# Kernel optimization log

Hardware: AMD Instinct MI355X
Metric: run time of the kernel (lower is better)

Reference implementation:

```python
import jax, jax.numpy as jnp
import numpy as np

BN_EPS = 1e-5


def cond_conv(x, att_w, att_b, weight, pad):
    """CondConv: per-sample expert-mixed conv.
    x: [N,C,H,W]; att_w: [K,C]; att_b: [K]; weight: [K,O,I,kh,kw]; pad: (ph,pw)."""
    pooled = x.mean(axis=(2, 3))                         # [N,C]  (AdaptiveAvgPool2d(1))
    att = jax.nn.sigmoid(pooled @ att_w.T + att_b)       # [N,K]  (1x1 conv + sigmoid)
    agg_w = jnp.einsum('nk,koihw->noihw', att, weight)   # per-sample kernels [N,O,I,kh,kw]

    def conv1(xi, wi):
        return jax.lax.conv_general_dilated(
            xi[None], wi, window_strides=(1, 1),
            padding=[(pad[0], pad[0]), (pad[1], pad[1])],
            dimension_numbers=('NCHW', 'OIHW', 'NCHW'))[0]

    return jax.vmap(conv1)(x, agg_w)                     # [N,O,H,W]


def batchnorm(x, gamma, beta):
    # training-mode BN: biased batch stats over (N,H,W)
    mean = x.mean(axis=(0, 2, 3), keepdims=True)
    var = x.var(axis=(0, 2, 3), keepdims=True)
    xn = (x - mean) * jax.lax.rsqrt(var + BN_EPS)
    return xn * gamma[None, :, None, None] + beta[None, :, None, None]


def channel_shuffle(x, g):
    N, C, H, W = x.shape
    return x.reshape(N, g, C // g, H, W).transpose(0, 2, 1, 3, 4).reshape(N, C, H, W)


def setup_inputs() -> dict:
    key = jax.random.key(0)
    ks = jax.random.split(key, 8)
    N, C, H, W = 32, 256, 64, 64
    Cb, K = C // 4, 4
    inp = {
        'x': jax.random.normal(ks[0], (N, C, H, W), jnp.float32),
        'sq_att_w': jax.random.normal(ks[1], (K, Cb), jnp.float32) * 0.1,
        'sq_att_b': jnp.zeros((K,), jnp.float32),
        'sq_w': jax.random.normal(ks[2], (K, Cb, Cb, 3, 3), jnp.float32) * 0.05,
        'sq_g': jnp.ones((Cb,), jnp.float32),
        'sq_b': jnp.zeros((Cb,), jnp.float32),
        'ver_att_w': jax.random.normal(ks[3], (K, Cb), jnp.float32) * 0.1,
        'ver_att_b': jnp.zeros((K,), jnp.float32),
        'ver_w': jax.random.normal(ks[4], (K, Cb, Cb, 3, 1), jnp.float32) * 0.05,
        'ver_g': jnp.ones((Cb,), jnp.float32),
        'ver_b': jnp.zeros((Cb,), jnp.float32),
        'hor_att_w': jax.random.normal(ks[5], (K, Cb), jnp.float32) * 0.1,
        'hor_att_b': jnp.zeros((K,), jnp.float32),
        'hor_w': jax.random.normal(ks[6], (K, Cb, Cb, 1, 3), jnp.float32) * 0.05,
        'hor_g': jnp.ones((Cb,), jnp.float32),
        'hor_b': jnp.zeros((Cb,), jnp.float32),
    }
    return inp


def reference(x, sq_att_w, sq_att_b, sq_w, sq_g, sq_b,
              ver_att_w, ver_att_b, ver_w, ver_g, ver_b,
              hor_att_w, hor_att_b, hor_w, hor_g, hor_b):
    # q_Split: chunk into 4 along channels
    s0, s1, s2, s3 = jnp.split(x, 4, axis=1)
    # square branch: CondConv 3x3 pad 1 + BN
    sq = batchnorm(cond_conv(s1, sq_att_w, sq_att_b, sq_w, (1, 1)), sq_g, sq_b)
    # vertical branch: CondConv 3x1 pad (1,0) + BN (crop layer is Identity since offset=0)
    ve = batchnorm(cond_conv(s2, ver_att_w, ver_att_b, ver_w, (1, 0)), ver_g, ver_b)
    # horizontal branch: CondConv 1x3 pad (0,1) + BN
    ho = batchnorm(cond_conv(s3, hor_att_w, hor_att_b, hor_w, (0, 1)), hor_g, hor_b)
    out = jnp.concatenate((s0, sq, ve, ho), axis=1)
    return channel_shuffle(out, 8)
```

## Files before the change

### kernel.cpp

```cpp
#include <hip/hip_runtime.h>
#include <cstddef>
#include <cstdint>


typedef __attribute__((ext_vector_type(8))) short frag8;
typedef __attribute__((ext_vector_type(16))) float accf16;

#define HW 4096
#define CNT_INV (1.0f / 131072.0f)
#define CSTR 1056
#define RSTR 8448
#define XT_BR (32ull * 66 * 8448)

#define WS_POOLED 0
#define WS_SS     6528
#define WS_PST    6912
#define WS_WBF_SQ  203520
#define WS_WBF_VER 793344
#define WS_WBF_HOR 989952
#define WS_XT      1186560

__device__ __forceinline__ int shuf_ch(int c) { return ((c & 31) << 3) | (c >> 5); }

__device__ __forceinline__ unsigned bf16pair(float a, float b) {
    unsigned ua = __builtin_bit_cast(unsigned, a);
    unsigned ub = __builtin_bit_cast(unsigned, b);
    ua = (ua + 0x7fffu + ((ua >> 16) & 1u)) >> 16;
    ub = (ub + 0x7fffu + ((ub >> 16) & 1u)) >> 16;
    return ua | (ub << 16);
}

__device__ __forceinline__ void gload_lds16(const void* g, void* l) {
    __builtin_amdgcn_global_load_lds(
        (const __attribute__((address_space(1))) void*)g,
        (__attribute__((address_space(3))) void*)l, 16, 0, 0);
}

__global__ void __launch_bounds__(256) prepass_kernel(
    const float* __restrict__ x, unsigned char* __restrict__ xt,
    float* __restrict__ pooled) {
    const int bid = blockIdx.x;
    const int c8 = bid & 7;
    const int n = (bid >> 3) & 31;
    const int b = bid >> 8;
    const int tid = threadIdx.x;
    const int w = tid & 63, q = tid >> 6;
    const float* xb = x + (size_t)(n * 256 + 64 * (b + 1) + c8 * 8) * HW;
    unsigned char* xtb = xt + (size_t)b * XT_BR + (size_t)n * 66 * RSTR + c8 * CSTR;

    float ps[8] = {0.f, 0.f, 0.f, 0.f, 0.f, 0.f, 0.f, 0.f};
    for (int h = q; h < 64; h += 4) {
        float v[8];
#pragma unroll
        for (int j = 0; j < 8; ++j) v[j] = xb[(size_t)j * HW + h * 64 + w];
        unsigned pk[4];
#pragma unroll
        for (int j = 0; j < 4; ++j) pk[j] = bf16pair(v[2 * j], v[2 * j + 1]);
        *(uint4*)(xtb + (size_t)(h + 1) * RSTR + (w + 1) * 16) = *(uint4*)pk;
#pragma unroll
        for (int j = 0; j < 8; ++j) ps[j] += v[j];
    }
    for (int idx = tid; idx < 260; idx += 256) {
        int p, slot;
        if (idx < 66)       { p = 0;         slot = idx; }
        else if (idx < 132) { p = 65;        slot = idx - 66; }
        else if (idx < 196) { p = idx - 131; slot = 0; }
        else                { p = idx - 195; slot = 65; }
        *(uint4*)(xtb + (size_t)p * RSTR + slot * 16) = uint4{0, 0, 0, 0};
    }
    __shared__ float red[4][8];
#pragma unroll
    for (int j = 0; j < 8; ++j)
#pragma unroll
        for (int off = 32; off; off >>= 1) ps[j] += __shfl_down(ps[j], off, 64);
    if ((tid & 63) == 0)
#pragma unroll
        for (int j = 0; j < 8; ++j) red[q][j] = ps[j];
    __syncthreads();
    if (tid < 8)
        pooled[(b * 32 + n) * 64 + c8 * 8 + tid] =
            (red[0][tid] + red[1][tid] + red[2][tid] + red[3][tid]) * (1.f / 4096.f);
}

template <int TAPS>
__device__ __forceinline__ void aggbf_body(const float* __restrict__ w,
                                           const float* __restrict__ pooled_b,
                                           const float* __restrict__ aw,
                                           const float* __restrict__ ab,
                                           unsigned* __restrict__ wbf, int bid) {
    const int tid = threadIdx.x;
    int idx = bid * 256 + tid;
    int ip = idx & 31;
    int o  = (idx >> 5) & 63;
    int t  = (idx >> 11) % TAPS;
    int n  = (idx >> 11) / TAPS;

    __shared__ float satt[4];
    if (tid < 64) {
        float p = pooled_b[n * 64 + tid];
#pragma unroll
        for (int k = 0; k < 4; ++k) {
            float v = p * aw[k * 64 + tid];
#pragma unroll
            for (int off = 32; off; off >>= 1) v += __shfl_down(v, off, 64);
            if (tid == 0) satt[k] = 1.f / (1.f + expf(-(v + ab[k])));
        }
    }
    __syncthreads();
    const float a0 = satt[0], a1 = satt[1], a2 = satt[2], a3 = satt[3];

    constexpr int PS = 64 * 64 * TAPS;
    int base = (o * 64 + ip * 2) * TAPS + t;
    float v0 = a0*w[base] + a1*w[PS+base] + a2*w[2*PS+base] + a3*w[3*PS+base];
    int base1 = base + TAPS;
    float v1 = a0*w[base1] + a1*w[PS+base1] + a2*w[2*PS+base1] + a3*w[3*PS+base1];
    int f = ip >> 2, jj = ip & 3;
    wbf[(((n * TAPS + t) * 8 + f) * 64 + o) * 4 + jj] = bf16pair(v0, v1);
}

__global__ void __launch_bounds__(256) aggbf_all_kernel(
    const float* __restrict__ pooled,
    const float* __restrict__ aw0, const float* __restrict__ ab0,
    const float* __restrict__ aw1, const float* __restrict__ ab1,
    const float* __restrict__ aw2, const float* __restrict__ ab2,
    const float* __restrict__ sq_w, const float* __restrict__ ver_w,
    const float* __restrict__ hor_w,
    unsigned* __restrict__ wsq, unsigned* __restrict__ wver,
    unsigned* __restrict__ whor) {
    int bid = blockIdx.x;
    if (bid < 2304)
        aggbf_body<9>(sq_w, pooled, aw0, ab0, wsq, bid);
    else if (bid < 3072)
        aggbf_body<3>(ver_w, pooled + 2048, aw1, ab1, wver, bid - 2304);
    else
        aggbf_body<3>(hor_w, pooled + 4096, aw2, ab2, whor, bid - 3072);
}

#define LOADA(dst, tt) \
    _Pragma("unroll") for (int kk = 0; kk < 4; ++kk) { \
        dst[kk]     = wp[(tt) * 512 + kk * 128]; \
        dst[4 + kk] = wp[(tt) * 512 + kk * 128 + 32]; \
    }

#define TAPSTEP(tt, CUR) { \
    const int r_ = (tt) / KW, dw_ = (tt) % KW - PW; \
    const unsigned char* bp_ = xs + (rh * 2 + r_) * RSTR + hi * CSTR + \
                               (wcol + dw_ + 1) * 16; \
    _Pragma("unroll") for (int kk = 0; kk < 4; ++kk) { \
        frag8 b0 = *(const frag8*)(bp_ + kk * 2 * CSTR); \
        frag8 b1 = *(const frag8*)(bp_ + kk * 2 * CSTR + RSTR); \
        a00 = __builtin_amdgcn_mfma_f32_32x32x16_bf16(CUR[kk],     b0, a00, 0, 0, 0); \
        a10 = __builtin_amdgcn_mfma_f32_32x32x16_bf16(CUR[4 + kk], b0, a10, 0, 0, 0); \
        a01 = __builtin_amdgcn_mfma_f32_32x32x16_bf16(CUR[kk],     b1, a01, 0, 0, 0); \
        a11 = __builtin_amdgcn_mfma_f32_32x32x16_bf16(CUR[4 + kk], b1, a11, 0, 0, 0); \
    } }

template <int KH, int KW, int PH, int PW>
__device__ __forceinline__ void conv_body(
    const unsigned char* __restrict__ xt, const unsigned* __restrict__ wbf,
    float* __restrict__ out, float* __restrict__ pst, int cbase, int bid,
    unsigned char* xs, float (*red1)[2][2][16], float (*red2)[2][2][16]) {
    constexpr int TAPS = KH * KW;
    constexpr int HB = 4;
    constexpr int ROWS = HB + KH - 1;
    constexpr int TOT = ROWS * RSTR;
    constexpr int NCH = (TOT + 1023) >> 10;
    const int hb = bid & 15, n = bid >> 4;
    const int h0 = hb * HB;
    const int tid = threadIdx.x;
    const int lane = tid & 63;
    const int wv = tid >> 6;
    const int rh = wv >> 1, wn = wv & 1;
    const int l31 = lane & 31, hi = lane >> 5;
    const int wcol = wn * 32 + l31;

    {
        const unsigned char* src = xt +
            (size_t)(n * 66 + h0 + (KH == 1 ? 1 : 0)) * RSTR + lane * 16;
#pragma unroll
        for (int c = wv; c < NCH; c += 4)
            gload_lds16(src + (c << 10), xs + (c << 10));
    }

    const frag8* wp = (const frag8*)wbf + (size_t)n * TAPS * 512 + hi * 64 + l31;

    frag8 aA[8], aB[8];
    LOADA(aA, 0);
    __syncthreads();

    accf16 a00 = {}, a01 = {}, a10 = {}, a11 = {};
#pragma unroll
    for (int t = 0; t < TAPS; t += 2) {
        if (t + 1 < TAPS) LOADA(aB, t + 1);
        TAPSTEP(t, aA);
        if (t + 2 < TAPS) LOADA(aA, t + 2);
        if (t + 1 < TAPS) TAPSTEP(t + 1, aB);
    }

    {
        float* ob = out + (size_t)n * 256 * HW + (h0 + rh * 2) * 64 + wcol;
#pragma unroll
        for (int rg = 0; rg < 16; ++rg) {
            const int o = (rg & 3) + 8 * (rg >> 2) + 4 * hi;
            float* p0 = ob + (size_t)shuf_ch(cbase + o) * HW;
            p0[0]  = a00[rg];
            p0[64] = a01[rg];
            float* p1 = ob + (size_t)shuf_ch(cbase + 32 + o) * HW;
            p1[0]  = a10[rg];
            p1[64] = a11[rg];
        }
    }

#pragma unroll
    for (int rg = 0; rg < 16; ++rg) {
        float u1 = a00[rg] + a01[rg];
        float u2 = a00[rg] * a00[rg] + a01[rg] * a01[rg];
        float w1 = a10[rg] + a11[rg];
        float w2 = a10[rg] * a10[rg] + a11[rg] * a11[rg];
#pragma unroll
        for (int off = 16; off; off >>= 1) {
            u1 += __shfl_down(u1, off, 32);
            u2 += __shfl_down(u2, off, 32);
            w1 += __shfl_down(w1, off, 32);
            w2 += __shfl_down(w2, off, 32);
        }
        if (l31 == 0) {
            red1[wv][0][hi][rg] = u1; red2[wv][0][hi][rg] = u2;
            red1[wv][1][hi][rg] = w1; red2[wv][1][hi][rg] = w2;
        }
    }
    __syncthreads();
    if (tid < 64) {
        const int rg = tid & 15, hi2 = (tid >> 4) & 1, wm2 = tid >> 5;
        float s1 = 0.f, s2 = 0.f;
#pragma unroll
        for (int v = 0; v < 4; ++v) {
            s1 += red1[v][wm2][hi2][rg];
            s2 += red2[v][wm2][hi2][rg];
        }
        const int o = wm2 * 32 + (rg & 3) + 8 * (rg >> 2) + 4 * hi2;
        const int slot = n * 16 + hb;
        pst[o * 1024 + slot] = s1;
        pst[o * 1024 + 512 + slot] = s2;
    }
}

__device__ __forceinline__ void s0_body(const float* __restrict__ x,
                                        float* __restrict__ out, int bid) {
    const int n = bid >> 4, c0 = (bid & 15) * 4, tid = threadIdx.x;
#pragma unroll
    for (int j = 0; j < 4; ++j) {
        const int c = c0 + j;
        const float4* s = (const float4*)(x + (size_t)(n * 256 + c) * HW);
        float4* d = (float4*)(out + (size_t)(n * 256 + shuf_ch(c)) * HW);
#pragma unroll
        for (int it = 0; it < 4; ++it) d[tid + it * 256] = s[tid + it * 256];
    }
}

__global__ void __launch_bounds__(256, 3) conv_all_kernel(
    const float* __restrict__ x, const unsigned char* __restrict__ xt,
    const unsigned* __restrict__ wsq, const unsigned* __restrict__ wver,
    const unsigned* __restrict__ whor,
    float* __restrict__ out, float* __restrict__ pst) {
    __shared__ __align__(16) unsigned char xs[6 * RSTR + 512];
    __shared__ float red1[4][2][2][16], red2[4][2][2][16];
    int bid = blockIdx.x;
    if (bid < 512)
        conv_body<3, 3, 1, 1>(xt, wsq, out, pst, 64, bid, xs, red1, red2);
    else if (bid < 1024)
        conv_body<3, 1, 1, 0>(xt + XT_BR, wver, out, pst + 65536, 128,
                              bid - 512, xs, red1, red2);
    else if (bid < 1536)
        conv_body<1, 3, 0, 1>(xt + 2 * XT_BR, whor, out, pst + 131072, 192,
                              bid - 1024, xs, red1, red2);
    else
        s0_body(x, out, bid - 1536);
}

__global__ void __launch_bounds__(256) bnstats_all_kernel(
    const float* __restrict__ pst,
    const float* __restrict__ g0, const float* __restrict__ b0,
    const float* __restrict__ g1, const float* __restrict__ b1,
    const float* __restrict__ g2, const float* __restrict__ b2,
    float* __restrict__ ss) {
    int br = blockIdx.x >> 6, o = blockIdx.x & 63, t = threadIdx.x;
    const float* gamma = (br == 0) ? g0 : (br == 1) ? g1 : g2;
    const float* beta  = (br == 0) ? b0 : (br == 1) ? b1 : b2;
    const float* p = pst + br * 65536 + o * 1024;
    float s1 = 0.f, s2 = 0.f;
    for (int i = t; i < 512; i += 256) {
        s1 += p[i];
        s2 += p[512 + i];
    }
#pragma unroll
    for (int off = 32; off; off >>= 1) {
        s1 += __shfl_down(s1, off, 64);
        s2 += __shfl_down(s2, off, 64);
    }
    __shared__ float r1[4], r2[4];
    if ((t & 63) == 0) { r1[t >> 6] = s1; r2[t >> 6] = s2; }
    __syncthreads();
    if (t == 0) {
        float S1 = r1[0] + r1[1] + r1[2] + r1[3];
        float S2 = r2[0] + r2[1] + r2[2] + r2[3];
        float mean = S1 * CNT_INV;
        float var = S2 * CNT_INV - mean * mean;
        float scale = rsqrtf(var + 1e-5f) * gamma[o];
        ss[br * 128 + o * 2 + 0] = scale;
        ss[br * 128 + o * 2 + 1] = beta[o] - mean * scale;
    }
}

__global__ void __launch_bounds__(256) bn_all_kernel(float* __restrict__ out,
                                                     const float* __restrict__ ss) {
    int gbid = blockIdx.x;
    int sub = gbid >> 13;
    int bid = gbid & 8191;
    int chunk = bid & 3;
    int n = (bid >> 2) & 31;
    int o = bid >> 7;
    float scale = ss[sub * 128 + o * 2], shift = ss[sub * 128 + o * 2 + 1];
    int c_out = shuf_ch(64 * (sub + 1) + o);
    float4* p = (float4*)(out + (size_t)(n * 256 + c_out) * HW) + chunk * 256 + threadIdx.x;
    float4 v = *p;
    v.x = fmaf(v.x, scale, shift);
    v.y = fmaf(v.y, scale, shift);
    v.z = fmaf(v.z, scale, shift);
    v.w = fmaf(v.w, scale, shift);
    *p = v;
}

extern "C" void kernel_launch(void* const* d_in, const int* in_sizes, int n_in,
                              void* d_out, int out_size, void* d_ws, size_t ws_size,
                              hipStream_t stream) {
    const float* x        = (const float*)d_in[0];
    const float* sq_att_w = (const float*)d_in[1];
    const float* sq_att_b = (const float*)d_in[2];
    const float* sq_w     = (const float*)d_in[3];
    const float* sq_g     = (const float*)d_in[4];
    const float* sq_b     = (const float*)d_in[5];
    const float* ver_att_w= (const float*)d_in[6];
    const float* ver_att_b= (const float*)d_in[7];
    const float* ver_w    = (const float*)d_in[8];
    const float* ver_g    = (const float*)d_in[9];
    const float* ver_b    = (const float*)d_in[10];
    const float* hor_att_w= (const float*)d_in[11];
    const float* hor_att_b= (const float*)d_in[12];
    const float* hor_w    = (const float*)d_in[13];
    const float* hor_g    = (const float*)d_in[14];
    const float* hor_b    = (const float*)d_in[15];
    float* out = (float*)d_out;
    float* ws = (float*)d_ws;

    float* pooled = ws + WS_POOLED;
    float* ss     = ws + WS_SS;
    float* pst    = ws + WS_PST;
    unsigned* wbf_sq  = (unsigned*)(ws + WS_WBF_SQ);
    unsigned* wbf_ver = (unsigned*)(ws + WS_WBF_VER);
    unsigned* wbf_hor = (unsigned*)(ws + WS_WBF_HOR);
    unsigned char* xt = (unsigned char*)(ws + WS_XT);

    prepass_kernel<<<768, 256, 0, stream>>>(x, xt, pooled);
    aggbf_all_kernel<<<3840, 256, 0, stream>>>(pooled,
                                               sq_att_w, sq_att_b,
                                               ver_att_w, ver_att_b,
                                               hor_att_w, hor_att_b,
                                               sq_w, ver_w, hor_w,
                                               wbf_sq, wbf_ver, wbf_hor);
    conv_all_kernel<<<2048, 256, 0, stream>>>(x, xt, wbf_sq, wbf_ver, wbf_hor,
                                              out, pst);
    bnstats_all_kernel<<<192, 256, 0, stream>>>(pst, sq_g, sq_b, ver_g, ver_b,
                                                hor_g, hor_b, ss);
    bn_all_kernel<<<24576, 256, 0, stream>>>(out, ss);
}
```

Baseline: 156.2 us.

## Store conv outputs as bf16 intermediate, move s0 copy into prepass, interleave conv blocks

The convolution now writes raw outputs as bf16 to a workspace buffer instead of fp32 into the final output. The BN apply kernel reads that bf16 buffer and writes normalized fp32 to the shuffled output, replacing a read-modify-write of fp32 data. The s0 passthrough copy moves from the conv kernel into the prepass, and conv block indices are remapped so the three branches interleave across the grid. BN statistics still come from fp32 accumulators, but the values being normalized are rounded to bf16 first, which adds rounding error to the output.

```diff
diff --git a/kernel.cpp b/kernel.cpp
--- a/kernel.cpp
+++ b/kernel.cpp
@@ -19,6 +19,7 @@
 #define WS_WBF_VER 793344
 #define WS_WBF_HOR 989952
 #define WS_XT      1186560
+#define WS_CVOUT   14568448
 
 __device__ __forceinline__ int shuf_ch(int c) { return ((c & 31) << 3) | (c >> 5); }
 
@@ -30,6 +31,18 @@
     return ua | (ub << 16);
 }
 
+__device__ __forceinline__ unsigned short bf16r(float a) {
+    unsigned ua = __builtin_bit_cast(unsigned, a);
+    return (unsigned short)((ua + 0x7fffu + ((ua >> 16) & 1u)) >> 16);
+}
+
+__device__ __forceinline__ float bf16lo(unsigned u) {
+    return __builtin_bit_cast(float, u << 16);
+}
+__device__ __forceinline__ float bf16hi(unsigned u) {
+    return __builtin_bit_cast(float, u & 0xffff0000u);
+}
+
 __device__ __forceinline__ void gload_lds16(const void* g, void* l) {
     __builtin_amdgcn_global_load_lds(
         (const __attribute__((address_space(1))) void*)g,
@@ -38,12 +51,27 @@
 
 __global__ void __launch_bounds__(256) prepass_kernel(
     const float* __restrict__ x, unsigned char* __restrict__ xt,
-    float* __restrict__ pooled) {
+    float* __restrict__ pooled, float* __restrict__ out) {
     const int bid = blockIdx.x;
+    const int tid = threadIdx.x;
+
+    if (bid >= 768) {
+        const int sid = bid - 768;
+        const int c8 = sid & 7, n = sid >> 3;
+#pragma unroll
+        for (int j = 0; j < 8; ++j) {
+            const int c = c8 * 8 + j;
+            const float4* s = (const float4*)(x + (size_t)(n * 256 + c) * HW);
+            float4* d = (float4*)(out + (size_t)(n * 256 + shuf_ch(c)) * HW);
+#pragma unroll
+            for (int it = 0; it < 4; ++it) d[tid + it * 256] = s[tid + it * 256];
+        }
+        return;
+    }
+
     const int c8 = bid & 7;
     const int n = (bid >> 3) & 31;
     const int b = bid >> 8;
-    const int tid = threadIdx.x;
     const int w = tid & 63, q = tid >> 6;
     const float* xb = x + (size_t)(n * 256 + 64 * (b + 1) + c8 * 8) * HW;
     unsigned char* xtb = xt + (size_t)b * XT_BR + (size_t)n * 66 * RSTR + c8 * CSTR;
@@ -158,8 +186,9 @@
 template <int KH, int KW, int PH, int PW>
 __device__ __forceinline__ void conv_body(
     const unsigned char* __restrict__ xt, const unsigned* __restrict__ wbf,
-    float* __restrict__ out, float* __restrict__ pst, int cbase, int bid,
-    unsigned char* xs, float (*red1)[2][2][16], float (*red2)[2][2][16]) {
+    unsigned short* __restrict__ cvout, float* __restrict__ pst, int cbase,
+    int bid, unsigned char* xs, float (*red1)[2][2][16],
+    float (*red2)[2][2][16]) {
     constexpr int TAPS = KH * KW;
     constexpr int HB = 4;
     constexpr int ROWS = HB + KH - 1;
@@ -198,16 +227,17 @@
     }
 
     {
-        float* ob = out + (size_t)n * 256 * HW + (h0 + rh * 2) * 64 + wcol;
+        unsigned short* cb = cvout + (size_t)(n * 192 + (cbase - 64)) * HW +
+                             (h0 + rh * 2) * 64 + wcol;
 #pragma unroll
         for (int rg = 0; rg < 16; ++rg) {
             const int o = (rg & 3) + 8 * (rg >> 2) + 4 * hi;
-            float* p0 = ob + (size_t)shuf_ch(cbase + o) * HW;
-            p0[0]  = a00[rg];
-            p0[64] = a01[rg];
-            float* p1 = ob + (size_t)shuf_ch(cbase + 32 + o) * HW;
-            p1[0]  = a10[rg];
-            p1[64] = a11[rg];
+            unsigned short* p0 = cb + (size_t)o * HW;
+            p0[0]  = bf16r(a00[rg]);
+            p0[64] = bf16r(a01[rg]);
+            unsigned short* p1 = cb + (size_t)(o + 32) * HW;
+            p1[0]  = bf16r(a10[rg]);
+            p1[64] = bf16r(a11[rg]);
         }
     }
 
@@ -245,37 +275,22 @@
     }
 }
 
-__device__ __forceinline__ void s0_body(const float* __restrict__ x,
-                                        float* __restrict__ out, int bid) {
-    const int n = bid >> 4, c0 = (bid & 15) * 4, tid = threadIdx.x;
-#pragma unroll
-    for (int j = 0; j < 4; ++j) {
-        const int c = c0 + j;
-        const float4* s = (const float4*)(x + (size_t)(n * 256 + c) * HW);
-        float4* d = (float4*)(out + (size_t)(n * 256 + shuf_ch(c)) * HW);
-#pragma unroll
-        for (int it = 0; it < 4; ++it) d[tid + it * 256] = s[tid + it * 256];
-    }
-}
-
 __global__ void __launch_bounds__(256, 3) conv_all_kernel(
-    const float* __restrict__ x, const unsigned char* __restrict__ xt,
+    const unsigned char* __restrict__ xt,
     const unsigned* __restrict__ wsq, const unsigned* __restrict__ wver,
     const unsigned* __restrict__ whor,
-    float* __restrict__ out, float* __restrict__ pst) {
+    unsigned short* __restrict__ cvout, float* __restrict__ pst) {
     __shared__ __align__(16) unsigned char xs[6 * RSTR + 512];
     __shared__ float red1[4][2][2][16], red2[4][2][2][16];
-    int bid = blockIdx.x;
+    int bid = (blockIdx.x & 7) * 192 + (blockIdx.x >> 3);
     if (bid < 512)
-        conv_body<3, 3, 1, 1>(xt, wsq, out, pst, 64, bid, xs, red1, red2);
+        conv_body<3, 3, 1, 1>(xt, wsq, cvout, pst, 64, bid, xs, red1, red2);
     else if (bid < 1024)
-        conv_body<3, 1, 1, 0>(xt + XT_BR, wver, out, pst + 65536, 128,
+        conv_body<3, 1, 1, 0>(xt + XT_BR, wver, cvout, pst + 65536, 128,
                               bid - 512, xs, red1, red2);
-    else if (bid < 1536)
-        conv_body<1, 3, 0, 1>(xt + 2 * XT_BR, whor, out, pst + 131072, 192,
+    else
+        conv_body<1, 3, 0, 1>(xt + 2 * XT_BR, whor, cvout, pst + 131072, 192,
                               bid - 1024, xs, red1, red2);
-    else
-        s0_body(x, out, bid - 1536);
 }
 
 __global__ void __launch_bounds__(256) bnstats_all_kernel(
@@ -312,23 +327,31 @@
     }
 }
 
-__global__ void __launch_bounds__(256) bn_all_kernel(float* __restrict__ out,
-                                                     const float* __restrict__ ss) {
-    int gbid = blockIdx.x;
-    int sub = gbid >> 13;
-    int bid = gbid & 8191;
-    int chunk = bid & 3;
-    int n = (bid >> 2) & 31;
-    int o = bid >> 7;
+__global__ void __launch_bounds__(256) bn_all_kernel(
+    const unsigned short* __restrict__ cvout, float* __restrict__ out,
+    const float* __restrict__ ss) {
+    int g = blockIdx.x;
+    int half = g & 1;
+    int n = (g >> 1) & 31;
+    int o = (g >> 6) & 63;
+    int sub = g >> 12;
     float scale = ss[sub * 128 + o * 2], shift = ss[sub * 128 + o * 2 + 1];
-    int c_out = shuf_ch(64 * (sub + 1) + o);
-    float4* p = (float4*)(out + (size_t)(n * 256 + c_out) * HW) + chunk * 256 + threadIdx.x;
-    float4 v = *p;
-    v.x = fmaf(v.x, scale, shift);
-    v.y = fmaf(v.y, scale, shift);
-    v.z = fmaf(v.z, scale, shift);
-    v.w = fmaf(v.w, scale, shift);
-    *p = v;
+    const uint4* src = (const uint4*)(cvout +
+        (size_t)(n * 192 + sub * 64 + o) * HW + half * 2048) + threadIdx.x;
+    float* dst = out + (size_t)(n * 256 + shuf_ch(64 * (sub + 1) + o)) * HW +
+                 half * 2048 + threadIdx.x * 8;
+    uint4 r = *src;
+    float4 f0, f1;
+    f0.x = fmaf(bf16lo(r.x), scale, shift);
+    f0.y = fmaf(bf16hi(r.x), scale, shift);
+    f0.z = fmaf(bf16lo(r.y), scale, shift);
+    f0.w = fmaf(bf16hi(r.y), scale, shift);
+    f1.x = fmaf(bf16lo(r.z), scale, shift);
+    f1.y = fmaf(bf16hi(r.z), scale, shift);
+    f1.z = fmaf(bf16lo(r.w), scale, shift);
+    f1.w = fmaf(bf16hi(r.w), scale, shift);
+    *(float4*)dst = f0;
+    *(float4*)(dst + 4) = f1;
 }
 
 extern "C" void kernel_launch(void* const* d_in, const int* in_sizes, int n_in,
@@ -360,17 +383,18 @@
     unsigned* wbf_ver = (unsigned*)(ws + WS_WBF_VER);
     unsigned* wbf_hor = (unsigned*)(ws + WS_WBF_HOR);
     unsigned char* xt = (unsigned char*)(ws + WS_XT);
-
-    prepass_kernel<<<768, 256, 0, stream>>>(x, xt, pooled);
+    unsigned short* cvout = (unsigned short*)(ws + WS_CVOUT);
+
+    prepass_kernel<<<1024, 256, 0, stream>>>(x, xt, pooled, out);
     aggbf_all_kernel<<<3840, 256, 0, stream>>>(pooled,
                                                sq_att_w, sq_att_b,
                                                ver_att_w, ver_att_b,
                                                hor_att_w, hor_att_b,
                                                sq_w, ver_w, hor_w,
                                                wbf_sq, wbf_ver, wbf_hor);
-    conv_all_kernel<<<2048, 256, 0, stream>>>(x, xt, wbf_sq, wbf_ver, wbf_hor,
-                                              out, pst);
+    conv_all_kernel<<<1536, 256, 0, stream>>>(xt, wbf_sq, wbf_ver, wbf_hor,
+                                              cvout, pst);
     bnstats_all_kernel<<<192, 256, 0, stream>>>(pst, sq_g, sq_b, ver_g, ver_b,
                                                 hor_g, hor_b, ss);
-    bn_all_kernel<<<24576, 256, 0, stream>>>(out, ss);
-}
+    bn_all_kernel<<<12288, 256, 0, stream>>>(cvout, out, ss);
+}
```

Measured after the change: 161.7 us. 3.6% more time.
